# Kernel tuning notes

Measured on AMD Instinct MI355X. Metric: run time of the kernel, lower is better.

Reference implementation:

```python
import jax, jax.numpy as jnp
import numpy as np

N = 100000   # nodes
H = 4        # heads
C = 32       # out feats per head (= n_classes)
E = 1600000  # edges
IN = 256     # in feats
NEG_SLOPE = 0.2


def setup_inputs() -> dict:
    key = jax.random.key(0)
    ks = jax.random.split(key, 7)
    x = jax.random.normal(ks[0], (N, IN), dtype=jnp.float32)
    src = jax.random.randint(ks[1], (E,), 0, N, dtype=jnp.int32)
    dst = jax.random.randint(ks[2], (E,), 0, N, dtype=jnp.int32)
    # Xavier-ish scaling for stability
    W = jax.random.normal(ks[3], (IN, H * C), dtype=jnp.float32) / np.sqrt(IN)
    attn_l = jax.random.normal(ks[4], (H, C), dtype=jnp.float32) / np.sqrt(C)
    attn_r = jax.random.normal(ks[5], (H, C), dtype=jnp.float32) / np.sqrt(C)
    bias = jnp.zeros((H * C,), dtype=jnp.float32)
    return {"x": x, "src": src, "dst": dst, "W": W,
            "attn_l": attn_l, "attn_r": attn_r, "bias": bias}


def reference(x, src, dst, W, attn_l, attn_r, bias):
    # GATConv: project, per-edge attention score, edge-softmax over dst, scatter-agg
    feat = (x @ W).reshape(N, H, C)                       # [N,H,C]
    el = jnp.einsum('nhc,hc->nh', feat, attn_l)           # [N,H]
    er = jnp.einsum('nhc,hc->nh', feat, attn_r)           # [N,H]
    e = jax.nn.leaky_relu(el[src] + er[dst], NEG_SLOPE)   # [E,H]
    # numerically-stable segment softmax over incoming edges of each dst node
    m = jax.ops.segment_max(e, dst, num_segments=N)       # [N,H]
    ex = jnp.exp(e - m[dst])                              # [E,H]
    s = jax.ops.segment_sum(ex, dst, num_segments=N)      # [N,H]
    alpha = ex / s[dst]                                   # [E,H]
    # weighted scatter-aggregate of source features
    msg = alpha[:, :, None] * feat[src]                   # [E,H,C]
    out = jax.ops.segment_sum(msg, dst, num_segments=N)   # [N,H,C]
    out = out + bias.reshape(1, H, C)
    h = out.mean(axis=1)                                  # mean over heads -> [N,C]
    return jax.nn.relu(h)
```

## Files before the change

### kernel.cpp

```cpp
#include <hip/hip_runtime.h>
#include <hip/hip_fp16.h>
#include <cstdint>

#define N_NODES 100000
#define H_HEADS 4
#define C_FEATS 32
#define HC 128
#define E_EDGES 1600000
#define IN_F 256
#define NEG_SLOPE 0.2f

#define BSHIFT 7
#define NBUCK 782
#define NREG 8
#define CAPB8 384
#define PH1_CHUNK 4096
#define PH1_BLOCKS ((E_EDGES + PH1_CHUNK - 1) / PH1_CHUNK)
#define GEMM_BLOCKS ((N_NODES + 127) / 128)
#define HALFCAP 1408
#define SWCAP 384
#define PADW 264

typedef _Float16 half8 __attribute__((ext_vector_type(8)));
typedef _Float16 half4v __attribute__((ext_vector_type(4)));
typedef float f32x4 __attribute__((ext_vector_type(4)));
typedef int i32x4 __attribute__((ext_vector_type(4)));

__global__ __launch_bounds__(256) void prep_w(const float* __restrict__ W,
                                              _Float16* __restrict__ W16t,
                                              int* __restrict__ gcnt) {
    int c = blockIdx.x;
    int k = threadIdx.x;
    W16t[c * IN_F + k] = (_Float16)W[k * HC + c];
    if (c == 0)
        for (int i = k; i < NREG * NBUCK; i += 256) gcnt[i] = 0;
}

__global__ __launch_bounds__(256) void gemm_bucket(const float* __restrict__ x,
                                                   const _Float16* __restrict__ W16t,
                                                   const float* __restrict__ attn_l,
                                                   const float* __restrict__ attn_r,
                                                   const int* __restrict__ src,
                                                   const int* __restrict__ dst,
                                                   _Float16* __restrict__ feat16,
                                                   float* __restrict__ el,
                                                   float* __restrict__ er,
                                                   int* __restrict__ gcnt,
                                                   unsigned* __restrict__ bucket) {
    __shared__ int hist[NBUCK];
    __shared__ _Float16 xs[128 * PADW];
    const int t = threadIdx.x;

    if (blockIdx.x < PH1_BLOCKS) {
        const int rg    = blockIdx.x & (NREG - 1);
        const int base  = blockIdx.x * PH1_CHUNK;
        const int cnt_e = min(PH1_CHUNK, E_EDGES - base);
        for (int i = t; i < NBUCK; i += 256) hist[i] = 0;
        __syncthreads();

        unsigned w[16]; int bk[16];
        const i32x4* d4 = (const i32x4*)(dst + base);
        const i32x4* s4 = (const i32x4*)(src + base);
        #pragma unroll
        for (int j4 = 0; j4 < 4; ++j4) {
            int idx = t + j4 * 256;
            int e0  = idx * 4;
            if (e0 + 3 < cnt_e) {
                i32x4 d = d4[idx];
                i32x4 s = s4[idx];
                #pragma unroll
                for (int k = 0; k < 4; ++k) {
                    int jj = j4 * 4 + k;
                    bk[jj] = d[k] >> BSHIFT;
                    w[jj] = ((unsigned)(d[k] & ((1 << BSHIFT) - 1)) << 24) | (unsigned)s[k];
                    atomicAdd(&hist[bk[jj]], 1);
                }
            } else {
                #pragma unroll
                for (int k = 0; k < 4; ++k) {
                    int jj = j4 * 4 + k;
                    bk[jj] = -1;
                    if (e0 + k < cnt_e) {
                        int dj = dst[base + e0 + k];
                        int sj = src[base + e0 + k];
                        bk[jj] = dj >> BSHIFT;
                        w[jj] = ((unsigned)(dj & ((1 << BSHIFT) - 1)) << 24) | (unsigned)sj;
                        atomicAdd(&hist[bk[jj]], 1);
                    }
                }
            }
        }
        __syncthreads();
        for (int i = t; i < NBUCK; i += 256) {
            int c = hist[i];
            hist[i] = (c > 0) ? atomicAdd(&gcnt[rg * NBUCK + i], c) : 0;
        }
        __syncthreads();
        #pragma unroll
        for (int j = 0; j < 16; ++j) {
            if (bk[j] >= 0) {
                int slot = atomicAdd(&hist[bk[j]], 1);
                if (slot < CAPB8)
                    bucket[((size_t)rg * NBUCK + bk[j]) * CAPB8 + slot] = w[j];
            }
        }
        return;
    }

    const int blk = blockIdx.x - PH1_BLOCKS;

    #pragma unroll
    for (int i = 0; i < 32; ++i) {
        int q   = i * 256 + t;
        int row = q >> 6;
        int c4  = q & 63;
        int gr  = blk * 128 + row;
        int r   = gr < N_NODES ? gr : N_NODES - 1;
        f32x4 v = __builtin_nontemporal_load(
            (const f32x4*)&x[(size_t)r * IN_F + c4 * 4]);
        half4v hv;
        hv[0] = (_Float16)v[0]; hv[1] = (_Float16)v[1];
        hv[2] = (_Float16)v[2]; hv[3] = (_Float16)v[3];
        *(half4v*)&xs[row * PADW + c4 * 4] = hv;
    }
    __syncthreads();

    const int w    = t >> 6;
    const int lane = t & 63;
    const int lrow = lane & 15;
    const int kq   = lane >> 4;
    const int row0 = w * 32 + lrow;
    const int gr0  = blk * 128 + row0;
    const int gr1  = gr0 + 16;

    f32x4 acc0[8], acc1[8];
    #pragma unroll
    for (int c = 0; c < 8; ++c) {
        acc0[c] = (f32x4){0.f, 0.f, 0.f, 0.f};
        acc1[c] = (f32x4){0.f, 0.f, 0.f, 0.f};
    }

    #pragma unroll
    for (int s = 0; s < 8; ++s) {
        const int k0 = s * 32 + kq * 8;
        half8 af0 = *(const half8*)&xs[row0 * PADW + k0];
        half8 af1 = *(const half8*)&xs[(row0 + 16) * PADW + k0];
        #pragma unroll
        for (int c = 0; c < 8; ++c) {
            half8 bf = *(const half8*)&W16t[(size_t)(c * 16 + lrow) * IN_F + k0];
            acc0[c] = __builtin_amdgcn_mfma_f32_16x16x32_f16(bf, af0, acc0[c], 0, 0, 0);
            acc1[c] = __builtin_amdgcn_mfma_f32_16x16x32_f16(bf, af1, acc1[c], 0, 0, 0);
        }
    }

    #pragma unroll
    for (int tile = 0; tile < 2; ++tile) {
        const int gr = tile == 0 ? gr0 : gr1;
        f32x4* acc = tile == 0 ? acc0 : acc1;
        float pl[4] = {0.f, 0.f, 0.f, 0.f}, pr[4] = {0.f, 0.f, 0.f, 0.f};
        #pragma unroll
        for (int c = 0; c < 8; ++c) {
            const int h = c >> 1;
            #pragma unroll
            for (int j = 0; j < 4; ++j) {
                const int col = c * 16 + kq * 4 + j;
                pl[h] += acc[c][j] * attn_l[col];
                pr[h] += acc[c][j] * attn_r[col];
            }
        }
        #pragma unroll
        for (int h = 0; h < 4; ++h) {
            pl[h] += __shfl_xor(pl[h], 16, 64); pl[h] += __shfl_xor(pl[h], 32, 64);
            pr[h] += __shfl_xor(pr[h], 16, 64); pr[h] += __shfl_xor(pr[h], 32, 64);
        }
        if (gr < N_NODES) {
            #pragma unroll
            for (int c = 0; c < 8; ++c) {
                half4v hv;
                hv[0] = (_Float16)acc[c][0]; hv[1] = (_Float16)acc[c][1];
                hv[2] = (_Float16)acc[c][2]; hv[3] = (_Float16)acc[c][3];
                *(half4v*)&feat16[(size_t)gr * HC + c * 16 + kq * 4] = hv;
            }
            if (kq == 0) {
                *(float4*)&el[gr * 4] = make_float4(pl[0], pl[1], pl[2], pl[3]);
                *(float4*)&er[gr * 4] = make_float4(pr[0], pr[1], pr[2], pr[3]);
            }
        }
    }
}

__global__ __launch_bounds__(256) void gat_gather(const int* __restrict__ gcnt,
                                                  const unsigned* __restrict__ bucket,
                                                  const float* __restrict__ el,
                                                  const float* __restrict__ er,
                                                  const _Float16* __restrict__ feat16,
                                                  const float* __restrict__ bias,
                                                  float* __restrict__ out) {
    __shared__ int      cnt[64];
    __shared__ int      off[64];
    __shared__ int      lcsr[HALFCAP];
    __shared__ unsigned s_w[4][SWCAP][2];

    const int b   = blockIdx.x >> 1;
    const int sub = blockIdx.x & 1;
    const int t   = threadIdx.x;
    const int n0  = (b << BSHIFT) + sub * 64;

    if (t < 64) cnt[t] = 0;
    __syncthreads();
    #pragma unroll
    for (int rr = 0; rr < NREG; ++rr) {
        const int m = min(gcnt[rr * NBUCK + b], CAPB8);
        const size_t rbase = ((size_t)rr * NBUCK + b) * CAPB8;
        for (int i = t; i < m; i += 256) {
            unsigned wrd = bucket[rbase + i];
            int nb = wrd >> 24;
            if ((nb >> 6) == sub) atomicAdd(&cnt[nb & 63], 1);
        }
    }
    __syncthreads();
    if (t < 64) {
        int v = cnt[t];
        int inc = v;
        #pragma unroll
        for (int o = 1; o < 64; o <<= 1) {
            int u = __shfl_up(inc, o, 64);
            if (t >= o) inc += u;
        }
        off[t] = inc - v;
        cnt[t] = 0;
    }
    __syncthreads();
    #pragma unroll
    for (int rr = 0; rr < NREG; ++rr) {
        const int m = min(gcnt[rr * NBUCK + b], CAPB8);
        const size_t rbase = ((size_t)rr * NBUCK + b) * CAPB8;
        for (int i = t; i < m; i += 256) {
            unsigned wrd = bucket[rbase + i];
            int nb = wrd >> 24;
            if ((nb >> 6) == sub) {
                int r = atomicAdd(&cnt[nb & 63], 1);
                int p = off[nb & 63] + r;
                if (p < HALFCAP) lcsr[p] = (int)(wrd & 0xBFFFFFFFu);
            }
        }
    }
    __syncthreads();

    const int wv   = t >> 6;
    const int lane = t & 63;
    const int q    = lane >> 4;
    const int ql   = lane & 15;
    const int h    = ql >> 2;

    const int wbase = off[wv * 16];
    const int wlast = wv * 16 + 15;
    const int nE    = min(off[wlast] + cnt[wlast] - wbase, SWCAP);
    for (int i = lane; i < nE; i += 64) {
        int wrd = lcsr[wbase + i];
        int s   = wrd & 0xFFFFFF;
        int nl  = (wrd >> 24) & 63;
        float4 a  = *(const float4*)&el[(size_t)s * 4];
        float4 bb = *(const float4*)&er[(size_t)(n0 + nl) * 4];
        float v0 = a.x + bb.x, v1 = a.y + bb.y, v2 = a.z + bb.z, v3 = a.w + bb.w;
        v0 = fmaxf(v0, NEG_SLOPE * v0); v1 = fmaxf(v1, NEG_SLOPE * v1);
        v2 = fmaxf(v2, NEG_SLOPE * v2); v3 = fmaxf(v3, NEG_SLOPE * v3);
        __half2 p01 = __floats2half2_rn(__expf(v0), __expf(v1));
        __half2 p23 = __floats2half2_rn(__expf(v2), __expf(v3));
        s_w[wv][i][0] = *(unsigned*)&p01;
        s_w[wv][i][1] = *(unsigned*)&p23;
    }
    __builtin_amdgcn_sched_barrier(0);

    float bv[8];
    #pragma unroll
    for (int k = 0; k < 8; ++k) bv[k] = bias[h * C_FEATS + (ql & 3) * 8 + k];

    for (int r0 = 0; r0 < 16; r0 += 4) {
        const int nl   = wv * 16 + r0 + q;
        const int n    = n0 + nl;
        const int bofs = off[nl];
        const int widx = bofs - wbase;
        int dg = cnt[nl];
        dg = min(dg, SWCAP - widx);
        if (dg < 0 || n >= N_NODES) dg = 0;

        float ac[8] = {0.f, 0.f, 0.f, 0.f, 0.f, 0.f, 0.f, 0.f};
        float sh = 0.f;
        #pragma unroll 4
        for (int j = 0; j < dg; ++j) {
            unsigned pw = s_w[wv][widx + j][h >> 1];
            __half2 hp = *(__half2*)&pw;
            float wgt = (h & 1) ? __high2float(hp) : __low2float(hp);
            int s = lcsr[bofs + j] & 0xFFFFFF;
            half8 f = *(const half8*)&feat16[(size_t)s * HC + ql * 8];
            #pragma unroll
            for (int k = 0; k < 8; ++k) ac[k] += wgt * (float)f[k];
            if ((ql & 3) == 0) sh += wgt;
        }
        __builtin_amdgcn_sched_barrier(0);

        float d = __shfl(sh, (lane & 48) | (ql & 12), 64);
        float inv = d > 0.f ? 1.f / d : 0.f;
        float o[8];
        #pragma unroll
        for (int k = 0; k < 8; ++k) o[k] = ac[k] * inv + bv[k];
        #pragma unroll
        for (int k = 0; k < 8; ++k) {
            o[k] += __shfl_xor(o[k], 4, 64);
            o[k] += __shfl_xor(o[k], 8, 64);
        }
        if (n < N_NODES && ql < 4) {
            float4 r1, r2;
            r1.x = fmaxf(o[0] * 0.25f, 0.f); r1.y = fmaxf(o[1] * 0.25f, 0.f);
            r1.z = fmaxf(o[2] * 0.25f, 0.f); r1.w = fmaxf(o[3] * 0.25f, 0.f);
            r2.x = fmaxf(o[4] * 0.25f, 0.f); r2.y = fmaxf(o[5] * 0.25f, 0.f);
            r2.z = fmaxf(o[6] * 0.25f, 0.f); r2.w = fmaxf(o[7] * 0.25f, 0.f);
            *(float4*)&out[(size_t)n * C_FEATS + ql * 8]     = r1;
            *(float4*)&out[(size_t)n * C_FEATS + ql * 8 + 4] = r2;
        }
    }
}

extern "C" void kernel_launch(void* const* d_in, const int* in_sizes, int n_in,
                              void* d_out, int out_size, void* d_ws, size_t ws_size,
                              hipStream_t stream) {
    const float* x      = (const float*)d_in[0];
    const int*   src    = (const int*)d_in[1];
    const int*   dst    = (const int*)d_in[2];
    const float* W      = (const float*)d_in[3];
    const float* attn_l = (const float*)d_in[4];
    const float* attn_r = (const float*)d_in[5];
    const float* bias   = (const float*)d_in[6];
    float* out = (float*)d_out;

    char* ws = (char*)d_ws;
    const size_t FEAT16_B = (size_t)N_NODES * HC * 2;
    const size_t NH_B     = (size_t)N_NODES * H_HEADS * 4;
    size_t off = 0;
    _Float16* feat16 = (_Float16*)(ws + off); off += FEAT16_B;
    float* el        = (float*)(ws + off);    off += NH_B;
    float* er        = (float*)(ws + off);    off += NH_B;
    _Float16* W16t   = (_Float16*)(ws + off); off += (size_t)HC * IN_F * 2;
    int*   gcnt      = (int*)(ws + off);      off += (size_t)NREG * NBUCK * 4;
    off = (off + 255) & ~(size_t)255;
    unsigned* bucket = (unsigned*)(ws + off); off += (size_t)NREG * NBUCK * CAPB8 * 4;

    prep_w<<<HC, IN_F, 0, stream>>>(W, W16t, gcnt);
    gemm_bucket<<<PH1_BLOCKS + GEMM_BLOCKS, 256, 0, stream>>>(
        x, W16t, attn_l, attn_r, src, dst, feat16, el, er, gcnt, bucket);
    gat_gather<<<NBUCK * 2, 256, 0, stream>>>(gcnt, bucket, el, er,
                                              feat16, bias, out);
}
```

Baseline: 144.6 us.

## Double-buffer x tiles along K in GEMM to overlap loads with MFMA

The GEMM blocks used to stage the whole 128x256 x tile in LDS before any MFMA work. Now K is split into four chunks of 64, with two LDS buffers: the next chunk is loaded into registers while MFMAs run on the current one, then converted and stored. The histogram and tile buffers are unioned into one shared array. LDS use falls from about 67KB to about 37KB, which should allow more blocks per CU, at the cost of extra barriers per K step.

```diff
diff --git a/kernel.cpp b/kernel.cpp
--- a/kernel.cpp
+++ b/kernel.cpp
@@ -19,7 +19,8 @@
 #define GEMM_BLOCKS ((N_NODES + 127) / 128)
 #define HALFCAP 1408
 #define SWCAP 384
-#define PADW 264
+#define BK 64
+#define PADK 72
 
 typedef _Float16 half8 __attribute__((ext_vector_type(8)));
 typedef _Float16 half4v __attribute__((ext_vector_type(4)));
@@ -47,11 +48,11 @@
                                                    float* __restrict__ er,
                                                    int* __restrict__ gcnt,
                                                    unsigned* __restrict__ bucket) {
-    __shared__ int hist[NBUCK];
-    __shared__ _Float16 xs[128 * PADW];
+    __shared__ __align__(16) char smem[2 * 128 * PADK * 2];
     const int t = threadIdx.x;
 
     if (blockIdx.x < PH1_BLOCKS) {
+        int* hist = (int*)smem;
         const int rg    = blockIdx.x & (NREG - 1);
         const int base  = blockIdx.x * PH1_CHUNK;
         const int cnt_e = min(PH1_CHUNK, E_EDGES - base);
@@ -107,24 +108,8 @@
         return;
     }
 
-    const int blk = blockIdx.x - PH1_BLOCKS;
-
-    #pragma unroll
-    for (int i = 0; i < 32; ++i) {
-        int q   = i * 256 + t;
-        int row = q >> 6;
-        int c4  = q & 63;
-        int gr  = blk * 128 + row;
-        int r   = gr < N_NODES ? gr : N_NODES - 1;
-        f32x4 v = __builtin_nontemporal_load(
-            (const f32x4*)&x[(size_t)r * IN_F + c4 * 4]);
-        half4v hv;
-        hv[0] = (_Float16)v[0]; hv[1] = (_Float16)v[1];
-        hv[2] = (_Float16)v[2]; hv[3] = (_Float16)v[3];
-        *(half4v*)&xs[row * PADW + c4 * 4] = hv;
-    }
-    __syncthreads();
-
+    _Float16* xs = (_Float16*)smem;
+    const int blk  = blockIdx.x - PH1_BLOCKS;
     const int w    = t >> 6;
     const int lane = t & 63;
     const int lrow = lane & 15;
@@ -133,6 +118,24 @@
     const int gr0  = blk * 128 + row0;
     const int gr1  = gr0 + 16;
 
+    f32x4 ld[8];
+    #pragma unroll
+    for (int i = 0; i < 8; ++i) {
+        int q = i * 256 + t, row = q >> 4, c4 = q & 15;
+        int gr = blk * 128 + row;
+        int r  = gr < N_NODES ? gr : N_NODES - 1;
+        ld[i] = __builtin_nontemporal_load((const f32x4*)&x[(size_t)r * IN_F + c4 * 4]);
+    }
+    #pragma unroll
+    for (int i = 0; i < 8; ++i) {
+        int q = i * 256 + t, row = q >> 4, c4 = q & 15;
+        half4v hv;
+        hv[0] = (_Float16)ld[i][0]; hv[1] = (_Float16)ld[i][1];
+        hv[2] = (_Float16)ld[i][2]; hv[3] = (_Float16)ld[i][3];
+        *(half4v*)&xs[row * PADK + c4 * 4] = hv;
+    }
+    __syncthreads();
+
     f32x4 acc0[8], acc1[8];
     #pragma unroll
     for (int c = 0; c < 8; ++c) {
@@ -141,15 +144,42 @@
     }
 
     #pragma unroll
-    for (int s = 0; s < 8; ++s) {
-        const int k0 = s * 32 + kq * 8;
-        half8 af0 = *(const half8*)&xs[row0 * PADW + k0];
-        half8 af1 = *(const half8*)&xs[(row0 + 16) * PADW + k0];
-        #pragma unroll
-        for (int c = 0; c < 8; ++c) {
-            half8 bf = *(const half8*)&W16t[(size_t)(c * 16 + lrow) * IN_F + k0];
-            acc0[c] = __builtin_amdgcn_mfma_f32_16x16x32_f16(bf, af0, acc0[c], 0, 0, 0);
-            acc1[c] = __builtin_amdgcn_mfma_f32_16x16x32_f16(bf, af1, acc1[c], 0, 0, 0);
+    for (int s = 0; s < 4; ++s) {
+        const int buf = s & 1;
+        if (s < 3) {
+            #pragma unroll
+            for (int i = 0; i < 8; ++i) {
+                int q = i * 256 + t, row = q >> 4, c4 = q & 15;
+                int gr = blk * 128 + row;
+                int r  = gr < N_NODES ? gr : N_NODES - 1;
+                ld[i] = __builtin_nontemporal_load(
+                    (const f32x4*)&x[(size_t)r * IN_F + (s + 1) * BK + c4 * 4]);
+            }
+        }
+        #pragma unroll
+        for (int kk = 0; kk < 2; ++kk) {
+            const int kl = kk * 32 + kq * 8;
+            const int kg = s * BK + kl;
+            half8 af0 = *(const half8*)&xs[buf * (128 * PADK) + row0 * PADK + kl];
+            half8 af1 = *(const half8*)&xs[buf * (128 * PADK) + (row0 + 16) * PADK + kl];
+            #pragma unroll
+            for (int c = 0; c < 8; ++c) {
+                half8 bf = *(const half8*)&W16t[(size_t)(c * 16 + lrow) * IN_F + kg];
+                acc0[c] = __builtin_amdgcn_mfma_f32_16x16x32_f16(bf, af0, acc0[c], 0, 0, 0);
+                acc1[c] = __builtin_amdgcn_mfma_f32_16x16x32_f16(bf, af1, acc1[c], 0, 0, 0);
+            }
+        }
+        if (s < 3) {
+            __syncthreads();
+            #pragma unroll
+            for (int i = 0; i < 8; ++i) {
+                int q = i * 256 + t, row = q >> 4, c4 = q & 15;
+                half4v hv;
+                hv[0] = (_Float16)ld[i][0]; hv[1] = (_Float16)ld[i][1];
+                hv[2] = (_Float16)ld[i][2]; hv[3] = (_Float16)ld[i][3];
+                *(half4v*)&xs[(buf ^ 1) * (128 * PADK) + row * PADK + c4 * 4] = hv;
+            }
+            __syncthreads();
         }
     }
 
```

Result: slower. 147.6 us (+2.1%).
